# Kernel tuning notes

Hardware: AMD Instinct MI355X
Metric: run time of the kernel (lower is better)

## Reference

```python
import jax, jax.numpy as jnp
import numpy as np

H = 16
D = 64  # head_dim = 1024 // 16
SCALE = D ** -0.5


def setup_inputs() -> dict:
    key = jax.random.key(0)
    ks = jax.random.split(key, 12)
    B, N, C = 2, 2048, 1024
    s = C ** -0.5
    return {
        "hidden_states": jax.random.normal(ks[0], (B, N, C), jnp.float32),
        "pos_embeds": jax.random.normal(ks[1], (B, N, C), jnp.float32),
        "Wq": jax.random.normal(ks[2], (C, C), jnp.float32) * s,
        "bq": jnp.zeros((C,), jnp.float32),
        "Wk": jax.random.normal(ks[3], (C, C), jnp.float32) * s,
        "bk": jnp.zeros((C,), jnp.float32),
        "Wv": jax.random.normal(ks[4], (C, C), jnp.float32) * s,
        "bv": jnp.zeros((C,), jnp.float32),
        "Wpos": jax.random.normal(ks[5], (C, C), jnp.float32) * s,
        "pos_bias_u": jax.random.normal(ks[6], (H, D), jnp.float32) * 0.1,
        "pos_bias_v": jax.random.normal(ks[7], (H, D), jnp.float32) * 0.1,
        "Wo": jax.random.normal(ks[8], (C, C), jnp.float32) * s,
        "bo": jnp.zeros((C,), jnp.float32),
    }


def reference(hidden_states, pos_embeds, Wq, bq, Wk, bk, Wv, bv, Wpos,
              pos_bias_u, pos_bias_v, Wo, bo):
    B, N, C = hidden_states.shape
    # projections (torch Linear: y = x @ W.T + b), split heads -> (B, N, H, D)
    q = (hidden_states @ Wq.T + bq).reshape(B, N, H, D)
    k = (hidden_states @ Wk.T + bk).reshape(B, N, H, D)
    v = (hidden_states @ Wv.T + bv).reshape(B, N, H, D)
    p = (pos_embeds @ Wpos.T).reshape(B, N, H, D)
    # relative-position biased logits: matrix_ac + matrix_bd
    q_u = q + pos_bias_u  # (B,N,H,D) + (H,D)
    q_v = q + pos_bias_v
    ac = jnp.einsum('bnhd,bmhd->bhnm', q_u, k)
    bd = jnp.einsum('bnhd,bmhd->bhnm', q_v, p)
    attn = jax.nn.softmax((ac + bd) * SCALE, axis=-1)  # (B,H,N,N)
    out = jnp.einsum('bhnm,bmhd->bnhd', attn, v).reshape(B, N, C)
    return out @ Wo.T + bo
```

## Files before the change

kernel.cpp:

```cpp
#include <hip/hip_runtime.h>
#include <hip/hip_bf16.h>


typedef short bf16x8 __attribute__((ext_vector_type(8)));
typedef float f32x4 __attribute__((ext_vector_type(4)));

#define BB 2
#define NN 2048
#define CC 1024
#define HH 16
#define DD 64
#define MM (BB * NN)
#define SC2E 0.18033688f

__device__ __forceinline__ unsigned short f2bf(float f) {
    union { float f; unsigned int u; } x; x.f = f;
    unsigned int r = x.u + 0x7FFFu + ((x.u >> 16) & 1u);
    return (unsigned short)(r >> 16);
}

__device__ __forceinline__ float bf2f(unsigned short s) {
    union { unsigned int u; float f; } x; x.u = ((unsigned int)s) << 16;
    return x.f;
}

__device__ __forceinline__ unsigned int pk2(float a, float b) {
    __hip_bfloat162 h = __float22bfloat162_rn(make_float2(a, b));
    unsigned int u; __builtin_memcpy(&u, &h, 4); return u;
}

typedef __attribute__((address_space(1))) const unsigned int* gas1_t;
typedef __attribute__((address_space(3))) unsigned int* las3_t;

__device__ __forceinline__ void gload_lds16(const unsigned short* g, unsigned short* l) {
    __builtin_amdgcn_global_load_lds((gas1_t)g, (las3_t)l, 16, 0, 0);
}

__global__ __launch_bounds__(256) void cast_f32_bf16(const float* __restrict__ src,
                                                     unsigned short* __restrict__ dst,
                                                     int n4) {
    int i = blockIdx.x * 256 + threadIdx.x;
    if (i >= n4) return;
    float4 v = ((const float4*)src)[i];
    union { unsigned short s[4]; uint2 u; } p;
    p.s[0] = f2bf(v.x); p.s[1] = f2bf(v.y); p.s[2] = f2bf(v.z); p.s[3] = f2bf(v.w);
    ((uint2*)dst)[i] = p.u;
}

template <int MODE>
__global__ __launch_bounds__(256) void gemm_bt(const unsigned short* __restrict__ A,
                                               const unsigned short* __restrict__ B,
                                               void* __restrict__ out0,
                                               const void* __restrict__ aux,
                                               const float* __restrict__ bias) {
    constexpr int K = CC;
    __shared__ unsigned short As[128 * 32];
    __shared__ unsigned short Bs[64 * 32];
    const int t = threadIdx.x;
    const int w = t >> 6, lane = t & 63, l15 = lane & 15, quad = lane >> 4;
    const int m0 = blockIdx.x * 128, n0 = blockIdx.y * 64;
    const int wm = (w >> 1) * 64, wn = (w & 1) * 32;

    f32x4 acc[4][2];
#pragma unroll
    for (int i = 0; i < 4; ++i)
#pragma unroll
        for (int j = 0; j < 2; ++j)
#pragma unroll
            for (int r = 0; r < 4; ++r) acc[i][j][r] = 0.f;

    for (int kb = 0; kb < K; kb += 32) {
        __syncthreads();
#pragma unroll
        for (int j = 0; j < 2; ++j) {
            int id = j * 256 + t;
            int row = id >> 2, c4 = id & 3;
            gload_lds16(&A[(size_t)(m0 + row) * K + kb + c4 * 8], &As[id * 8]);
        }
        {
            int row = t >> 2, c4 = t & 3;
            gload_lds16(&B[(size_t)(n0 + row) * K + kb + c4 * 8], &Bs[t * 8]);
        }
        __syncthreads();
        bf16x8 af[4], bfr[2];
#pragma unroll
        for (int i = 0; i < 4; ++i)
            af[i] = *(const bf16x8*)&As[(wm + i * 16 + l15) * 32 + quad * 8];
#pragma unroll
        for (int j = 0; j < 2; ++j)
            bfr[j] = *(const bf16x8*)&Bs[(wn + j * 16 + l15) * 32 + quad * 8];
#pragma unroll
        for (int i = 0; i < 4; ++i)
#pragma unroll
            for (int j = 0; j < 2; ++j)
                acc[i][j] = __builtin_amdgcn_mfma_f32_16x16x32_bf16(af[i], bfr[j], acc[i][j], 0, 0, 0);
    }

#pragma unroll
    for (int i = 0; i < 4; ++i) {
#pragma unroll
        for (int j = 0; j < 2; ++j) {
            const int col = n0 + wn + j * 16 + l15;
            const int row_base = m0 + wm + i * 16 + quad * 4;
            const float bc = (MODE == 4) ? 0.f : (bias ? bias[col] : 0.f);
            if (MODE == 0) {
#pragma unroll
                for (int r = 0; r < 4; ++r)
                    ((unsigned short*)out0)[(size_t)(row_base + r) * CC + col] = f2bf(acc[i][j][r] + bc);
            } else if (MODE == 1) {
#pragma unroll
                for (int r = 0; r < 4; ++r)
                    ((unsigned short*)out0)[(size_t)(row_base + r) * CC + col] =
                        f2bf((acc[i][j][r] + bc) * SC2E);
            } else if (MODE == 2) {
#pragma unroll
                for (int r = 0; r < 4; ++r)
                    ((float*)out0)[(size_t)(row_base + r) * CC + col] = acc[i][j][r] + bc;
            } else if (MODE == 4) {
#pragma unroll
                for (int r = 0; r < 4; ++r) {
                    float kv = bf2f(((const unsigned short*)aux)[(size_t)(row_base + r) * CC + col]);
                    ((unsigned short*)out0)[(size_t)(row_base + r) * CC + col] = f2bf(acc[i][j][r] + kv);
                }
            } else {
                const int b = row_base >> 11, nseq = row_base & 2047;
                const int hh = col >> 6, dd = col & 63;
                union { unsigned short s[4]; uint2 u; } pk;
#pragma unroll
                for (int r = 0; r < 4; ++r) pk.s[r] = f2bf(acc[i][j][r] + bc);
                size_t idx = ((size_t)(b * HH + hh) * DD + dd) * NN + nseq;
                *(uint2*)&((unsigned short*)out0)[idx] = pk.u;
            }
        }
    }
}

__global__ __launch_bounds__(256) void fuse_c(const unsigned short* __restrict__ k,
                                              const unsigned short* __restrict__ kp,
                                              const float* __restrict__ pbu,
                                              const float* __restrict__ pbv,
                                              float* __restrict__ c) {
    const int gw = (blockIdx.x * 256 + threadIdx.x) >> 6;
    const int lane = threadIdx.x & 63;
    const int row = gw >> 4, h = gw & 15;
    const size_t off = (size_t)row * CC + h * 64 + lane;
    const float u = pbu[h * 64 + lane], v = pbv[h * 64 + lane];
    float val = (u - v) * bf2f(k[off]) + v * bf2f(kp[off]);
#pragma unroll
    for (int o = 1; o < 64; o <<= 1) val += __shfl_xor(val, o);
    if (lane == 0) {
        const int b = row >> 11, n = row & 2047;
        c[((size_t)(b * HH + h)) * NN + n] = val * SC2E;
    }
}

#define PST 80
__global__ __launch_bounds__(256, 2) void attn_kernel(const unsigned short* __restrict__ q,
                                                      const unsigned short* __restrict__ kp,
                                                      const unsigned short* __restrict__ vt,
                                                      const float* __restrict__ cb,
                                                      unsigned short* __restrict__ att) {
    __shared__ unsigned short Ks[64 * 64];
    __shared__ unsigned short Vs[64 * 64];
    __shared__ unsigned short Ps[4][32 * PST];

    const int t = threadIdx.x;
    const int w = t >> 6, lane = t & 63, l15 = lane & 15, quad = lane >> 4;
    const int qt = blockIdx.x, h = blockIdx.y, b = blockIdx.z;
    const int sw = (l15 & 7) * 8;

    bf16x8 qf[2][2];
#pragma unroll
    for (int qb = 0; qb < 2; ++qb) {
        const int qrow = qt * 128 + w * 32 + qb * 16 + l15;
        const size_t qoff = ((size_t)(b * NN + qrow) * HH + h) * DD;
#pragma unroll
        for (int c2 = 0; c2 < 2; ++c2)
            qf[qb][c2] = *(const bf16x8*)&q[qoff + c2 * 32 + quad * 8];
    }

    f32x4 oT[4][2];
    float l_lane[2] = {0.f, 0.f};
#pragma unroll
    for (int db = 0; db < 4; ++db)
#pragma unroll
        for (int qb = 0; qb < 2; ++qb)
#pragma unroll
            for (int r = 0; r < 4; ++r) oT[db][qb][r] = 0.f;

    const size_t kbase = (size_t)b * NN * CC + (size_t)h * DD;
    const size_t vbase = (size_t)(b * HH + h) * DD * NN;
    const size_t cbase = (size_t)(b * HH + h) * NN;

    for (int kt = 0; kt < NN / 64; ++kt) {
        __syncthreads();
#pragma unroll
        for (int j = 0; j < 2; ++j) {
            int id = j * 256 + t, row = id >> 3, c8 = id & 7;
            int gc = (c8 ^ (row & 7)) * 8;
            gload_lds16(&kp[kbase + (size_t)(kt * 64 + row) * CC + gc], &Ks[id * 8]);
            gload_lds16(&vt[vbase + (size_t)row * NN + kt * 64 + gc], &Vs[id * 8]);
        }
        __syncthreads();

        f32x4 s[2][4];
#pragma unroll
        for (int t4 = 0; t4 < 4; ++t4) {
            f32x4 c4 = *(const f32x4*)&cb[cbase + kt * 64 + t4 * 16 + quad * 4];
            s[0][t4] = c4; s[1][t4] = c4;
        }
#pragma unroll
        for (int t4 = 0; t4 < 4; ++t4) {
            const int row = t4 * 16 + l15;
#pragma unroll
            for (int c2 = 0; c2 < 2; ++c2) {
                bf16x8 kf = *(const bf16x8*)&Ks[row * 64 + ((c2 * 4 + quad) * 8 ^ sw)];
#pragma unroll
                for (int qb = 0; qb < 2; ++qb)
                    s[qb][t4] = __builtin_amdgcn_mfma_f32_16x16x32_bf16(kf, qf[qb][c2], s[qb][t4], 0, 0, 0);
            }
        }

#pragma unroll
        for (int qb = 0; qb < 2; ++qb) {
            float rs = 0.f;
#pragma unroll
            for (int t4 = 0; t4 < 4; ++t4)
#pragma unroll
                for (int r = 0; r < 4; ++r) {
                    float pv = exp2f(s[qb][t4][r]);
                    s[qb][t4][r] = pv;
                    rs += pv;
                }
            l_lane[qb] += rs;
#pragma unroll
            for (int t4 = 0; t4 < 4; ++t4) {
                uint2 pk;
                pk.x = pk2(s[qb][t4][0], s[qb][t4][1]);
                pk.y = pk2(s[qb][t4][2], s[qb][t4][3]);
                *(uint2*)&Ps[w][(qb * 16 + l15) * PST + t4 * 16 + quad * 4] = pk;
            }
        }

#pragma unroll
        for (int c2 = 0; c2 < 2; ++c2) {
            bf16x8 pf[2];
#pragma unroll
            for (int qb = 0; qb < 2; ++qb)
                pf[qb] = *(const bf16x8*)&Ps[w][(qb * 16 + l15) * PST + c2 * 32 + quad * 8];
#pragma unroll
            for (int db = 0; db < 4; ++db) {
                bf16x8 vf = *(const bf16x8*)&Vs[(db * 16 + l15) * 64 + ((c2 * 4 + quad) * 8 ^ sw)];
#pragma unroll
                for (int qb = 0; qb < 2; ++qb)
                    oT[db][qb] = __builtin_amdgcn_mfma_f32_16x16x32_bf16(vf, pf[qb], oT[db][qb], 0, 0, 0);
            }
        }
    }

#pragma unroll
    for (int qb = 0; qb < 2; ++qb) {
        float l = l_lane[qb];
        l += __shfl_xor(l, 16);
        l += __shfl_xor(l, 32);
        const float inv = 1.f / l;
        const int qrow = qt * 128 + w * 32 + qb * 16 + l15;
        const size_t ob = ((size_t)(b * NN + qrow) * HH + h) * DD;
#pragma unroll
        for (int db = 0; db < 4; ++db) {
            uint2 pk;
            pk.x = pk2(oT[db][qb][0] * inv, oT[db][qb][1] * inv);
            pk.y = pk2(oT[db][qb][2] * inv, oT[db][qb][3] * inv);
            *(uint2*)&att[ob + db * 16 + quad * 4] = pk;
        }
    }
}

extern "C" void kernel_launch(void* const* d_in, const int* in_sizes, int n_in,
                              void* d_out, int out_size, void* d_ws, size_t ws_size,
                              hipStream_t stream) {
    const float* hs   = (const float*)d_in[0];
    const float* pos  = (const float*)d_in[1];
    const float* Wq   = (const float*)d_in[2];
    const float* bq   = (const float*)d_in[3];
    const float* Wk   = (const float*)d_in[4];
    const float* bk   = (const float*)d_in[5];
    const float* Wv   = (const float*)d_in[6];
    const float* bv   = (const float*)d_in[7];
    const float* Wpos = (const float*)d_in[8];
    const float* pbu  = (const float*)d_in[9];
    const float* pbv  = (const float*)d_in[10];
    const float* Wo   = (const float*)d_in[11];
    const float* bo   = (const float*)d_in[12];
    float* out = (float*)d_out;

    const size_t nHS = (size_t)MM * CC;
    const size_t nW  = (size_t)CC * CC;

    unsigned short* p = (unsigned short*)d_ws;
    unsigned short* hsb  = p;            p += nHS;
    unsigned short* posb = p;            p += nHS;
    unsigned short* wqb  = p;            p += nW;
    unsigned short* wkb  = p;            p += nW;
    unsigned short* wvb  = p;            p += nW;
    unsigned short* wpb  = p;            p += nW;
    unsigned short* wob  = p;            p += nW;
    unsigned short* qsb  = p;            p += nHS;
    unsigned short* kbf  = p;            p += nHS;
    unsigned short* kpb  = p;            p += nHS;
    unsigned short* vtb  = p;            p += nHS;
    float* cb = (float*)p;               p += (size_t)BB * HH * NN * 2;
    unsigned short* attb = hsb;

    cast_f32_bf16<<<(int)(nHS / 4 / 256), 256, 0, stream>>>(hs, hsb, (int)(nHS / 4));
    cast_f32_bf16<<<(int)(nHS / 4 / 256), 256, 0, stream>>>(pos, posb, (int)(nHS / 4));
    cast_f32_bf16<<<(int)(nW / 4 / 256), 256, 0, stream>>>(Wq, wqb, (int)(nW / 4));
    cast_f32_bf16<<<(int)(nW / 4 / 256), 256, 0, stream>>>(Wk, wkb, (int)(nW / 4));
    cast_f32_bf16<<<(int)(nW / 4 / 256), 256, 0, stream>>>(Wv, wvb, (int)(nW / 4));
    cast_f32_bf16<<<(int)(nW / 4 / 256), 256, 0, stream>>>(Wpos, wpb, (int)(nW / 4));
    cast_f32_bf16<<<(int)(nW / 4 / 256), 256, 0, stream>>>(Wo, wob, (int)(nW / 4));

    dim3 ggrid(MM / 128, CC / 64);
    gemm_bt<1><<<ggrid, 256, 0, stream>>>(hsb, wqb, qsb, nullptr, bq);
    gemm_bt<0><<<ggrid, 256, 0, stream>>>(hsb, wkb, kbf, nullptr, bk);
    gemm_bt<3><<<ggrid, 256, 0, stream>>>(hsb, wvb, vtb, nullptr, bv);
    gemm_bt<4><<<ggrid, 256, 0, stream>>>(posb, wpb, kpb, kbf, nullptr);

    fuse_c<<<MM * HH / 4, 256, 0, stream>>>(kbf, kpb, pbu, pbv, cb);

    dim3 agrid(NN / 128, HH, BB);
    attn_kernel<<<agrid, 256, 0, stream>>>(qsb, kpb, vtb, cb, attb);

    gemm_bt<2><<<ggrid, 256, 0, stream>>>(attb, wob, out, nullptr, bo);
}
```

Measured before the change: 301.5 us.

## Batch casts and QKVP GEMMs, enlarge GEMM tiles, shrink attention query tile

Merges the seven cast launches into one grid-indexed kernel and the four projection GEMMs into a single launch batched over blockIdx.z. GEMM tiles grow from 128x64 to 128x128, so each wave holds a 4x4 accumulator block and reuses each operand fragment more often. The k+p addition moves out of the P-projection epilogue into the fuse kernel, which now writes kp and the bias term together. The attention kernel processes 64 query rows per block instead of 128 and drops the occupancy hint, which doubles the grid but gives up reuse of K/V tiles across query sub-blocks. The risk is heavier register pressure in the larger GEMM tiles and the extra memory traffic of a separate pbf buffer.

```diff
diff --git a/kernel.cpp b/kernel.cpp
--- a/kernel.cpp
+++ b/kernel.cpp
@@ -36,36 +36,48 @@
     __builtin_amdgcn_global_load_lds((gas1_t)g, (las3_t)l, 16, 0, 0);
 }
 
-__global__ __launch_bounds__(256) void cast_f32_bf16(const float* __restrict__ src,
-                                                     unsigned short* __restrict__ dst,
-                                                     int n4) {
-    int i = blockIdx.x * 256 + threadIdx.x;
-    if (i >= n4) return;
-    float4 v = ((const float4*)src)[i];
-    union { unsigned short s[4]; uint2 u; } p;
-    p.s[0] = f2bf(v.x); p.s[1] = f2bf(v.y); p.s[2] = f2bf(v.z); p.s[3] = f2bf(v.w);
-    ((uint2*)dst)[i] = p.u;
-}
-
-template <int MODE>
-__global__ __launch_bounds__(256) void gemm_bt(const unsigned short* __restrict__ A,
-                                               const unsigned short* __restrict__ B,
-                                               void* __restrict__ out0,
-                                               const void* __restrict__ aux,
-                                               const float* __restrict__ bias) {
+struct CastArgs {
+    const float* src[7];
+    unsigned short* dst[7];
+    int n4[7];
+};
+__global__ __launch_bounds__(256) void cast_all(CastArgs a) {
+    const int seg = blockIdx.y;
+    const int i = blockIdx.x * 256 + threadIdx.x;
+    if (i >= a.n4[seg]) return;
+    float4 v = ((const float4*)a.src[seg])[i];
+    uint2 u;
+    u.x = pk2(v.x, v.y);
+    u.y = pk2(v.z, v.w);
+    ((uint2*)a.dst[seg])[i] = u;
+}
+
+struct GemmBatch {
+    const unsigned short* A[4];
+    const unsigned short* B[4];
+    unsigned short* out[4];
+    const float* bias[4];
+};
+__global__ __launch_bounds__(256) void gemm_qkvp(GemmBatch g) {
     constexpr int K = CC;
+    const int z = blockIdx.z;
+    const unsigned short* __restrict__ A = g.A[z];
+    const unsigned short* __restrict__ B = g.B[z];
+    unsigned short* __restrict__ out = g.out[z];
+    const float* __restrict__ bias = g.bias[z];
+
     __shared__ unsigned short As[128 * 32];
-    __shared__ unsigned short Bs[64 * 32];
+    __shared__ unsigned short Bs[128 * 32];
     const int t = threadIdx.x;
     const int w = t >> 6, lane = t & 63, l15 = lane & 15, quad = lane >> 4;
-    const int m0 = blockIdx.x * 128, n0 = blockIdx.y * 64;
-    const int wm = (w >> 1) * 64, wn = (w & 1) * 32;
-
-    f32x4 acc[4][2];
+    const int m0 = blockIdx.x * 128, n0 = blockIdx.y * 128;
+    const int wm = (w >> 1) * 64, wn = (w & 1) * 64;
+
+    f32x4 acc[4][4];
 #pragma unroll
     for (int i = 0; i < 4; ++i)
 #pragma unroll
-        for (int j = 0; j < 2; ++j)
+        for (int j = 0; j < 4; ++j)
 #pragma unroll
             for (int r = 0; r < 4; ++r) acc[i][j][r] = 0.f;
 
@@ -74,78 +86,130 @@
 #pragma unroll
         for (int j = 0; j < 2; ++j) {
             int id = j * 256 + t;
-            int row = id >> 2, c4 = id & 3;
-            gload_lds16(&A[(size_t)(m0 + row) * K + kb + c4 * 8], &As[id * 8]);
-        }
-        {
-            int row = t >> 2, c4 = t & 3;
-            gload_lds16(&B[(size_t)(n0 + row) * K + kb + c4 * 8], &Bs[t * 8]);
-        }
-        __syncthreads();
-        bf16x8 af[4], bfr[2];
+            int row = id >> 2, c4 = (id & 3) * 8;
+            gload_lds16(&A[(size_t)(m0 + row) * K + kb + c4], &As[id * 8]);
+            gload_lds16(&B[(size_t)(n0 + row) * K + kb + c4], &Bs[id * 8]);
+        }
+        __syncthreads();
+        bf16x8 af[4], bfr[4];
 #pragma unroll
         for (int i = 0; i < 4; ++i)
             af[i] = *(const bf16x8*)&As[(wm + i * 16 + l15) * 32 + quad * 8];
 #pragma unroll
-        for (int j = 0; j < 2; ++j)
+        for (int j = 0; j < 4; ++j)
             bfr[j] = *(const bf16x8*)&Bs[(wn + j * 16 + l15) * 32 + quad * 8];
 #pragma unroll
         for (int i = 0; i < 4; ++i)
 #pragma unroll
-            for (int j = 0; j < 2; ++j)
+            for (int j = 0; j < 4; ++j)
                 acc[i][j] = __builtin_amdgcn_mfma_f32_16x16x32_bf16(af[i], bfr[j], acc[i][j], 0, 0, 0);
     }
 
 #pragma unroll
     for (int i = 0; i < 4; ++i) {
 #pragma unroll
-        for (int j = 0; j < 2; ++j) {
+        for (int j = 0; j < 4; ++j) {
             const int col = n0 + wn + j * 16 + l15;
             const int row_base = m0 + wm + i * 16 + quad * 4;
-            const float bc = (MODE == 4) ? 0.f : (bias ? bias[col] : 0.f);
-            if (MODE == 0) {
+            if (z == 0) {
+                const float bc = bias[col];
 #pragma unroll
                 for (int r = 0; r < 4; ++r)
-                    ((unsigned short*)out0)[(size_t)(row_base + r) * CC + col] = f2bf(acc[i][j][r] + bc);
-            } else if (MODE == 1) {
+                    out[(size_t)(row_base + r) * CC + col] = f2bf((acc[i][j][r] + bc) * SC2E);
+            } else if (z == 1) {
+                const float bc = bias[col];
 #pragma unroll
                 for (int r = 0; r < 4; ++r)
-                    ((unsigned short*)out0)[(size_t)(row_base + r) * CC + col] =
-                        f2bf((acc[i][j][r] + bc) * SC2E);
-            } else if (MODE == 2) {
-#pragma unroll
-                for (int r = 0; r < 4; ++r)
-                    ((float*)out0)[(size_t)(row_base + r) * CC + col] = acc[i][j][r] + bc;
-            } else if (MODE == 4) {
-#pragma unroll
-                for (int r = 0; r < 4; ++r) {
-                    float kv = bf2f(((const unsigned short*)aux)[(size_t)(row_base + r) * CC + col]);
-                    ((unsigned short*)out0)[(size_t)(row_base + r) * CC + col] = f2bf(acc[i][j][r] + kv);
-                }
-            } else {
+                    out[(size_t)(row_base + r) * CC + col] = f2bf(acc[i][j][r] + bc);
+            } else if (z == 2) {
+                const float bc = bias[col];
                 const int b = row_base >> 11, nseq = row_base & 2047;
                 const int hh = col >> 6, dd = col & 63;
                 union { unsigned short s[4]; uint2 u; } pk;
 #pragma unroll
                 for (int r = 0; r < 4; ++r) pk.s[r] = f2bf(acc[i][j][r] + bc);
                 size_t idx = ((size_t)(b * HH + hh) * DD + dd) * NN + nseq;
-                *(uint2*)&((unsigned short*)out0)[idx] = pk.u;
+                *(uint2*)&out[idx] = pk.u;
+            } else {
+#pragma unroll
+                for (int r = 0; r < 4; ++r)
+                    out[(size_t)(row_base + r) * CC + col] = f2bf(acc[i][j][r]);
             }
         }
     }
 }
 
-__global__ __launch_bounds__(256) void fuse_c(const unsigned short* __restrict__ k,
-                                              const unsigned short* __restrict__ kp,
-                                              const float* __restrict__ pbu,
-                                              const float* __restrict__ pbv,
-                                              float* __restrict__ c) {
+__global__ __launch_bounds__(256) void gemm_out(const unsigned short* __restrict__ A,
+                                                const unsigned short* __restrict__ B,
+                                                float* __restrict__ out,
+                                                const float* __restrict__ bias) {
+    constexpr int K = CC;
+    __shared__ unsigned short As[128 * 32];
+    __shared__ unsigned short Bs[128 * 32];
+    const int t = threadIdx.x;
+    const int w = t >> 6, lane = t & 63, l15 = lane & 15, quad = lane >> 4;
+    const int m0 = blockIdx.x * 128, n0 = blockIdx.y * 128;
+    const int wm = (w >> 1) * 64, wn = (w & 1) * 64;
+
+    f32x4 acc[4][4];
+#pragma unroll
+    for (int i = 0; i < 4; ++i)
+#pragma unroll
+        for (int j = 0; j < 4; ++j)
+#pragma unroll
+            for (int r = 0; r < 4; ++r) acc[i][j][r] = 0.f;
+
+    for (int kb = 0; kb < K; kb += 32) {
+        __syncthreads();
+#pragma unroll
+        for (int j = 0; j < 2; ++j) {
+            int id = j * 256 + t;
+            int row = id >> 2, c4 = (id & 3) * 8;
+            gload_lds16(&A[(size_t)(m0 + row) * K + kb + c4], &As[id * 8]);
+            gload_lds16(&B[(size_t)(n0 + row) * K + kb + c4], &Bs[id * 8]);
+        }
+        __syncthreads();
+        bf16x8 af[4], bfr[4];
+#pragma unroll
+        for (int i = 0; i < 4; ++i)
+            af[i] = *(const bf16x8*)&As[(wm + i * 16 + l15) * 32 + quad * 8];
+#pragma unroll
+        for (int j = 0; j < 4; ++j)
+            bfr[j] = *(const bf16x8*)&Bs[(wn + j * 16 + l15) * 32 + quad * 8];
+#pragma unroll
+        for (int i = 0; i < 4; ++i)
+#pragma unroll
+            for (int j = 0; j < 4; ++j)
+                acc[i][j] = __builtin_amdgcn_mfma_f32_16x16x32_bf16(af[i], bfr[j], acc[i][j], 0, 0, 0);
+    }
+
+#pragma unroll
+    for (int i = 0; i < 4; ++i) {
+#pragma unroll
+        for (int j = 0; j < 4; ++j) {
+            const int col = n0 + wn + j * 16 + l15;
+            const int row_base = m0 + wm + i * 16 + quad * 4;
+            const float bc = bias[col];
+#pragma unroll
+            for (int r = 0; r < 4; ++r)
+                out[(size_t)(row_base + r) * CC + col] = acc[i][j][r] + bc;
+        }
+    }
+}
+
+__global__ __launch_bounds__(256) void fuse_kpc(const unsigned short* __restrict__ k,
+                                                const unsigned short* __restrict__ pp,
+                                                const float* __restrict__ pbu,
+                                                const float* __restrict__ pbv,
+                                                unsigned short* __restrict__ kp,
+                                                float* __restrict__ c) {
     const int gw = (blockIdx.x * 256 + threadIdx.x) >> 6;
     const int lane = threadIdx.x & 63;
     const int row = gw >> 4, h = gw & 15;
     const size_t off = (size_t)row * CC + h * 64 + lane;
-    const float u = pbu[h * 64 + lane], v = pbv[h * 64 + lane];
-    float val = (u - v) * bf2f(k[off]) + v * bf2f(kp[off]);
+    const float kv = bf2f(k[off]), pv = bf2f(pp[off]);
+    kp[off] = f2bf(kv + pv);
+    float val = pbu[h * 64 + lane] * kv + pbv[h * 64 + lane] * pv;
 #pragma unroll
     for (int o = 1; o < 64; o <<= 1) val += __shfl_xor(val, o);
     if (lane == 0) {
@@ -155,38 +219,33 @@
 }
 
 #define PST 80
-__global__ __launch_bounds__(256, 2) void attn_kernel(const unsigned short* __restrict__ q,
-                                                      const unsigned short* __restrict__ kp,
-                                                      const unsigned short* __restrict__ vt,
-                                                      const float* __restrict__ cb,
-                                                      unsigned short* __restrict__ att) {
+__global__ __launch_bounds__(256) void attn_kernel(const unsigned short* __restrict__ q,
+                                                   const unsigned short* __restrict__ kp,
+                                                   const unsigned short* __restrict__ vt,
+                                                   const float* __restrict__ cb,
+                                                   unsigned short* __restrict__ att) {
     __shared__ unsigned short Ks[64 * 64];
     __shared__ unsigned short Vs[64 * 64];
-    __shared__ unsigned short Ps[4][32 * PST];
+    __shared__ unsigned short Ps[4][16 * PST];
 
     const int t = threadIdx.x;
     const int w = t >> 6, lane = t & 63, l15 = lane & 15, quad = lane >> 4;
     const int qt = blockIdx.x, h = blockIdx.y, b = blockIdx.z;
     const int sw = (l15 & 7) * 8;
 
-    bf16x8 qf[2][2];
-#pragma unroll
-    for (int qb = 0; qb < 2; ++qb) {
-        const int qrow = qt * 128 + w * 32 + qb * 16 + l15;
-        const size_t qoff = ((size_t)(b * NN + qrow) * HH + h) * DD;
-#pragma unroll
-        for (int c2 = 0; c2 < 2; ++c2)
-            qf[qb][c2] = *(const bf16x8*)&q[qoff + c2 * 32 + quad * 8];
-    }
-
-    f32x4 oT[4][2];
-    float l_lane[2] = {0.f, 0.f};
+    const int qrow = qt * 64 + w * 16 + l15;
+    const size_t qoff = ((size_t)(b * NN + qrow) * HH + h) * DD;
+    bf16x8 qf[2];
+#pragma unroll
+    for (int c2 = 0; c2 < 2; ++c2)
+        qf[c2] = *(const bf16x8*)&q[qoff + c2 * 32 + quad * 8];
+
+    f32x4 oT[4];
+    float l_lane = 0.f;
 #pragma unroll
     for (int db = 0; db < 4; ++db)
 #pragma unroll
-        for (int qb = 0; qb < 2; ++qb)
-#pragma unroll
-            for (int r = 0; r < 4; ++r) oT[db][qb][r] = 0.f;
+        for (int r = 0; r < 4; ++r) oT[db][r] = 0.f;
 
     const size_t kbase = (size_t)b * NN * CC + (size_t)h * DD;
     const size_t vbase = (size_t)(b * HH + h) * DD * NN;
@@ -203,76 +262,60 @@
         }
         __syncthreads();
 
-        f32x4 s[2][4];
-#pragma unroll
-        for (int t4 = 0; t4 < 4; ++t4) {
-            f32x4 c4 = *(const f32x4*)&cb[cbase + kt * 64 + t4 * 16 + quad * 4];
-            s[0][t4] = c4; s[1][t4] = c4;
-        }
+        f32x4 s[4];
+#pragma unroll
+        for (int t4 = 0; t4 < 4; ++t4)
+            s[t4] = *(const f32x4*)&cb[cbase + kt * 64 + t4 * 16 + quad * 4];
 #pragma unroll
         for (int t4 = 0; t4 < 4; ++t4) {
             const int row = t4 * 16 + l15;
 #pragma unroll
             for (int c2 = 0; c2 < 2; ++c2) {
                 bf16x8 kf = *(const bf16x8*)&Ks[row * 64 + ((c2 * 4 + quad) * 8 ^ sw)];
-#pragma unroll
-                for (int qb = 0; qb < 2; ++qb)
-                    s[qb][t4] = __builtin_amdgcn_mfma_f32_16x16x32_bf16(kf, qf[qb][c2], s[qb][t4], 0, 0, 0);
+                s[t4] = __builtin_amdgcn_mfma_f32_16x16x32_bf16(kf, qf[c2], s[t4], 0, 0, 0);
             }
         }
 
-#pragma unroll
-        for (int qb = 0; qb < 2; ++qb) {
-            float rs = 0.f;
-#pragma unroll
-            for (int t4 = 0; t4 < 4; ++t4)
-#pragma unroll
-                for (int r = 0; r < 4; ++r) {
-                    float pv = exp2f(s[qb][t4][r]);
-                    s[qb][t4][r] = pv;
-                    rs += pv;
-                }
-            l_lane[qb] += rs;
-#pragma unroll
-            for (int t4 = 0; t4 < 4; ++t4) {
-                uint2 pk;
-                pk.x = pk2(s[qb][t4][0], s[qb][t4][1]);
-                pk.y = pk2(s[qb][t4][2], s[qb][t4][3]);
-                *(uint2*)&Ps[w][(qb * 16 + l15) * PST + t4 * 16 + quad * 4] = pk;
+        float rs = 0.f;
+#pragma unroll
+        for (int t4 = 0; t4 < 4; ++t4)
+#pragma unroll
+            for (int r = 0; r < 4; ++r) {
+                float pv = exp2f(s[t4][r]);
+                s[t4][r] = pv;
+                rs += pv;
             }
+        l_lane += rs;
+#pragma unroll
+        for (int t4 = 0; t4 < 4; ++t4) {
+            uint2 pk;
+            pk.x = pk2(s[t4][0], s[t4][1]);
+            pk.y = pk2(s[t4][2], s[t4][3]);
+            *(uint2*)&Ps[w][l15 * PST + t4 * 16 + quad * 4] = pk;
         }
 
 #pragma unroll
         for (int c2 = 0; c2 < 2; ++c2) {
-            bf16x8 pf[2];
-#pragma unroll
-            for (int qb = 0; qb < 2; ++qb)
-                pf[qb] = *(const bf16x8*)&Ps[w][(qb * 16 + l15) * PST + c2 * 32 + quad * 8];
+            bf16x8 pf = *(const bf16x8*)&Ps[w][l15 * PST + c2 * 32 + quad * 8];
 #pragma unroll
             for (int db = 0; db < 4; ++db) {
                 bf16x8 vf = *(const bf16x8*)&Vs[(db * 16 + l15) * 64 + ((c2 * 4 + quad) * 8 ^ sw)];
-#pragma unroll
-                for (int qb = 0; qb < 2; ++qb)
-                    oT[db][qb] = __builtin_amdgcn_mfma_f32_16x16x32_bf16(vf, pf[qb], oT[db][qb], 0, 0, 0);
+                oT[db] = __builtin_amdgcn_mfma_f32_16x16x32_bf16(vf, pf, oT[db], 0, 0, 0);
             }
         }
     }
 
-#pragma unroll
-    for (int qb = 0; qb < 2; ++qb) {
-        float l = l_lane[qb];
-        l += __shfl_xor(l, 16);
-        l += __shfl_xor(l, 32);
-        const float inv = 1.f / l;
-        const int qrow = qt * 128 + w * 32 + qb * 16 + l15;
-        const size_t ob = ((size_t)(b * NN + qrow) * HH + h) * DD;
-#pragma unroll
-        for (int db = 0; db < 4; ++db) {
-            uint2 pk;
-            pk.x = pk2(oT[db][qb][0] * inv, oT[db][qb][1] * inv);
-            pk.y = pk2(oT[db][qb][2] * inv, oT[db][qb][3] * inv);
-            *(uint2*)&att[ob + db * 16 + quad * 4] = pk;
-        }
+    float l = l_lane;
+    l += __shfl_xor(l, 16);
+    l += __shfl_xor(l, 32);
+    const float inv = 1.f / l;
+    const size_t ob = ((size_t)(b * NN + qrow) * HH + h) * DD;
+#pragma unroll
+    for (int db = 0; db < 4; ++db) {
+        uint2 pk;
+        pk.x = pk2(oT[db][0] * inv, oT[db][1] * inv);
+        pk.y = pk2(oT[db][2] * inv, oT[db][3] * inv);
+        *(uint2*)&att[ob + db * 16 + quad * 4] = pk;
     }
 }
 
@@ -307,29 +350,36 @@
     unsigned short* wob  = p;            p += nW;
     unsigned short* qsb  = p;            p += nHS;
     unsigned short* kbf  = p;            p += nHS;
+    unsigned short* pbf  = p;            p += nHS;
     unsigned short* kpb  = p;            p += nHS;
     unsigned short* vtb  = p;            p += nHS;
     float* cb = (float*)p;               p += (size_t)BB * HH * NN * 2;
     unsigned short* attb = hsb;
 
-    cast_f32_bf16<<<(int)(nHS / 4 / 256), 256, 0, stream>>>(hs, hsb, (int)(nHS / 4));
-    cast_f32_bf16<<<(int)(nHS / 4 / 256), 256, 0, stream>>>(pos, posb, (int)(nHS / 4));
-    cast_f32_bf16<<<(int)(nW / 4 / 256), 256, 0, stream>>>(Wq, wqb, (int)(nW / 4));
-    cast_f32_bf16<<<(int)(nW / 4 / 256), 256, 0, stream>>>(Wk, wkb, (int)(nW / 4));
-    cast_f32_bf16<<<(int)(nW / 4 / 256), 256, 0, stream>>>(Wv, wvb, (int)(nW / 4));
-    cast_f32_bf16<<<(int)(nW / 4 / 256), 256, 0, stream>>>(Wpos, wpb, (int)(nW / 4));
-    cast_f32_bf16<<<(int)(nW / 4 / 256), 256, 0, stream>>>(Wo, wob, (int)(nW / 4));
-
-    dim3 ggrid(MM / 128, CC / 64);
-    gemm_bt<1><<<ggrid, 256, 0, stream>>>(hsb, wqb, qsb, nullptr, bq);
-    gemm_bt<0><<<ggrid, 256, 0, stream>>>(hsb, wkb, kbf, nullptr, bk);
-    gemm_bt<3><<<ggrid, 256, 0, stream>>>(hsb, wvb, vtb, nullptr, bv);
-    gemm_bt<4><<<ggrid, 256, 0, stream>>>(posb, wpb, kpb, kbf, nullptr);
-
-    fuse_c<<<MM * HH / 4, 256, 0, stream>>>(kbf, kpb, pbu, pbv, cb);
-
-    dim3 agrid(NN / 128, HH, BB);
+    CastArgs ca;
+    ca.src[0] = hs;   ca.dst[0] = hsb;  ca.n4[0] = (int)(nHS / 4);
+    ca.src[1] = pos;  ca.dst[1] = posb; ca.n4[1] = (int)(nHS / 4);
+    ca.src[2] = Wq;   ca.dst[2] = wqb;  ca.n4[2] = (int)(nW / 4);
+    ca.src[3] = Wk;   ca.dst[3] = wkb;  ca.n4[3] = (int)(nW / 4);
+    ca.src[4] = Wv;   ca.dst[4] = wvb;  ca.n4[4] = (int)(nW / 4);
+    ca.src[5] = Wpos; ca.dst[5] = wpb;  ca.n4[5] = (int)(nW / 4);
+    ca.src[6] = Wo;   ca.dst[6] = wob;  ca.n4[6] = (int)(nW / 4);
+    dim3 cgrid((unsigned)(nHS / 4 / 256), 7);
+    cast_all<<<cgrid, 256, 0, stream>>>(ca);
+
+    GemmBatch gb;
+    gb.A[0] = hsb;  gb.B[0] = wqb; gb.out[0] = qsb; gb.bias[0] = bq;
+    gb.A[1] = hsb;  gb.B[1] = wkb; gb.out[1] = kbf; gb.bias[1] = bk;
+    gb.A[2] = hsb;  gb.B[2] = wvb; gb.out[2] = vtb; gb.bias[2] = bv;
+    gb.A[3] = posb; gb.B[3] = wpb; gb.out[3] = pbf; gb.bias[3] = nullptr;
+    dim3 ggrid(MM / 128, CC / 128, 4);
+    gemm_qkvp<<<ggrid, 256, 0, stream>>>(gb);
+
+    fuse_kpc<<<MM * HH / 4, 256, 0, stream>>>(kbf, pbf, pbu, pbv, kpb, cb);
+
+    dim3 agrid(NN / 64, HH, BB);
     attn_kernel<<<agrid, 256, 0, stream>>>(qsb, kpb, vtb, cb, attb);
 
-    gemm_bt<2><<<ggrid, 256, 0, stream>>>(attb, wob, out, nullptr, bo);
-}
+    dim3 ogrid(MM / 128, CC / 128);
+    gemm_out<<<ogrid, 256, 0, stream>>>(attb, wob, out, bo);
+}
```

After: 278.7 us. 7.6% less time.
